# Kernel optimization log

Measured on AMD Instinct MI355X. Metric: run time of the kernel, lower is better.

Reference implementation:

```python
import jax, jax.numpy as jnp
import numpy as np

S = 14       # grid size
B = 2        # boxes per cell
C = 20       # classes
N_EL = B * 5 + C   # 30
L_COORD = 5.0
L_NOOBJ = 0.5
BATCH = 4096
NBOX = 16


def setup_inputs() -> dict:
    key = jax.random.key(0)
    k1, k2, k3, k4 = jax.random.split(key, 4)
    prediction = jax.random.uniform(k1, (BATCH, S * S * N_EL), dtype=jnp.float32)
    # well-formed ground-truth boxes: centers in (0.05,0.95), sizes in (0.02,0.3)
    cxcy = jax.random.uniform(k2, (BATCH, NBOX, 2), minval=0.05, maxval=0.95, dtype=jnp.float32)
    wh = jax.random.uniform(k3, (BATCH, NBOX, 2), minval=0.02, maxval=0.3, dtype=jnp.float32)
    boxes = jnp.concatenate([cxcy - wh / 2, cxcy + wh / 2], axis=-1)  # x1,y1,x2,y2
    classes = jax.random.randint(k4, (BATCH, NBOX), 0, C, dtype=jnp.int32)
    return {"prediction": prediction, "boxes": boxes, "classes": classes}


def _encode(boxes, classes):
    """Vectorized version of YoloLoss.encode: scatter boxes into SxS grid cells.
    Faithful detail: class one-hot goes to channel 9+class (the original's
    off-by-one: class 0 lands on the 2nd confidence channel)."""
    bsz, nbox = classes.shape
    cell = 1.0 / S
    xy1, xy2 = boxes[..., :2], boxes[..., 2:]
    wh = xy2 - xy1
    cxcy = (xy1 + xy2) / 2
    ij = jnp.clip(jnp.ceil(cxcy / cell) - 1, 0, S - 1)          # [b,nbox,2] (x,y)
    dxy = cxcy / cell - ij                                      # delta inside cell
    ij = ij.astype(jnp.int32)
    one = jnp.ones_like(wh[..., :1])
    zcls = jnp.zeros(classes.shape + (C,), dtype=boxes.dtype)
    # layout: [dxy, wh, conf, dxy, wh, conf, class one-hots]
    base = jnp.concatenate([dxy, wh, one, dxy, wh, one, zcls], axis=-1)  # [b,nbox,30]
    cls_oh = jax.nn.one_hot(classes + (B * 5 - 1), N_EL, dtype=boxes.dtype)  # index 9+class
    vec = jnp.maximum(base, cls_oh)
    flat_idx = (jnp.arange(bsz, dtype=jnp.int32)[:, None] * (S * S)
                + ij[..., 1] * S + ij[..., 0]).reshape(-1)      # row-major (y,x)
    target = jnp.zeros((bsz * S * S, N_EL), dtype=boxes.dtype)
    return target.at[flat_idx].set(vec.reshape(-1, N_EL))


def _pairwise_iou(a, b):
    """a,b: [N,B,4] -> iou [N,B(pred),B(target)] (corner-format jaccard, as in
    the original, applied to (dx,dy,w,h) rows verbatim)."""
    a4 = a[:, :, None, :]
    b4 = b[:, None, :, :]
    lt = jnp.maximum(a4[..., :2], b4[..., :2])
    rb = jnp.minimum(a4[..., 2:], b4[..., 2:])
    whi = jnp.clip(rb - lt, 0.0)
    inter = whi[..., 0] * whi[..., 1]
    area_a = (a4[..., 2] - a4[..., 0]) * (a4[..., 3] - a4[..., 1])
    area_b = (b4[..., 2] - b4[..., 0]) * (b4[..., 3] - b4[..., 1])
    union = area_a + area_b - inter
    return inter / jnp.where(union == 0, 1.0, union)


def reference(prediction, boxes, classes):
    target = _encode(boxes, classes)                       # [bsz*S*S, 30]
    pred = prediction.reshape(-1, N_EL)
    coord = target[:, 4] > 0                               # cells containing objects
    coordf = coord.astype(pred.dtype)
    noobjf = (target[:, 4] == 0).astype(pred.dtype)

    conf_idx = jnp.array([4, 9])
    noobj_loss = jnp.sum(noobjf[:, None] * (pred[:, conf_idx] - target[:, conf_idx]) ** 2)
    class_loss = jnp.sum(coordf[:, None] * (pred[:, B * 5:] - target[:, B * 5:]) ** 2)

    bp = pred[:, :B * 5].reshape(-1, B, 5)                 # [N,B,5]
    bt = target[:, :B * 5].reshape(-1, B, 5)

    iou = _pairwise_iou(bp[..., :4], bt[..., :4])          # [N,B,B]
    max_index = jnp.argmax(iou, axis=1)                    # best pred per target box
    response = (max_index[:, None, :] == jnp.arange(B)[None, :, None]).any(-1)  # [N,B]
    resp = response & coord[:, None]
    respf = resp.astype(pred.dtype)

    contain_loss = jnp.sum(respf * (bp[..., 4] - bt[..., 4]) ** 2)
    bt_wh = jnp.where(resp[..., None], bt[..., 2:4], 1.0)  # guard sqrt at masked cells
    loc_loss = jnp.sum(respf * (((bp[..., :2] - bt[..., :2]) ** 2).sum(-1)
                                + ((jnp.sqrt(bp[..., 2:4]) - jnp.sqrt(bt_wh)) ** 2).sum(-1)))

    return L_COORD * loc_loss + contain_loss + L_NOOBJ * noobj_loss + class_loss
```

## Files before the change

### kernel.cpp

```cpp
#include <hip/hip_runtime.h>


#define SGRID 14
#define CELLS 196
#define NEL 30
#define NBOX 16
#define PRED_PER_BATCH 5880
#define VEC_PER_ROW 1470
#define STREAM_ITERS 12
#define STREAM_TPB 256
#define STREAM_CHUNK (STREAM_ITERS * STREAM_TPB)
#define WIN_TILE (4 * CELLS + 4)

typedef float v4f __attribute__((ext_vector_type(4)));

__device__ __forceinline__ float channel_sq_terms(v4f v, int c0, int m0, int m1) {
    float loss = 0.0f;
    #pragma unroll
    for (int j = 0; j < 4; ++j) {
        int cj = c0 + j;
        bool str = cj >= 30;
        int cc = str ? cj - 30 : cj;
        int m  = str ? m1 : m0;
        unsigned amask = (m < 0) ? 0x210u : 0x3FFFFC00u;
        float scale    = (m < 0) ? 0.5f : 1.0f;
        float wgt = ((amask >> cc) & 1u) ? scale : 0.0f;
        loss = fmaf(wgt * v[j], v[j], loss);
    }
    return loss;
}

__global__ __launch_bounds__(256) void yolo_fused_kernel(
    const v4f*    __restrict__ pred4,
    const float4* __restrict__ boxes,
    const int*    __restrict__ classes,
    float* __restrict__ partials,
    int nvec, int nrows)
{
    __shared__ int   s_win[WIN_TILE];
    __shared__ float s_w4[4];

    const int tid = threadIdx.x;
    const int v0  = blockIdx.x * STREAM_CHUNK;
    const int r0  = v0 / VEC_PER_ROW;
    const float cellw = (float)(1.0 / 14.0);

    float4 bx; int cls = 0; bool has_box = false;
    int rr = tid >> 4, row = r0 + rr, k = tid & 15;
    if (tid < 4 * NBOX && row < nrows) {
        bx  = boxes[row * NBOX + k];
        cls = classes[row * NBOX + k];
        has_box = true;
    }
    #pragma unroll
    for (int i = 0; i < (WIN_TILE + STREAM_TPB - 1) / STREAM_TPB; ++i) {
        int idx = tid + i * STREAM_TPB;
        if (idx < WIN_TILE) s_win[idx] = -1;
    }
    __syncthreads();
    float dx, dy, bw, bh; int cell = 0;
    if (has_box) {
        bw = bx.z - bx.x;  bh = bx.w - bx.y;
        float cx = (bx.x + bx.z) * 0.5f, cy = (bx.y + bx.w) * 0.5f;
        float fx = cx / cellw, fy = cy / cellw;
        float fi = fminf(fmaxf(ceilf(fx) - 1.0f, 0.0f), 13.0f);
        float fj = fminf(fmaxf(ceilf(fy) - 1.0f, 0.0f), 13.0f);
        dx = fx - fi;  dy = fy - fj;
        cell = (int)fj * SGRID + (int)fi;
        atomicMax(&s_win[rr * CELLS + cell], (k << 8) | (9 + cls));
    }
    __syncthreads();

    const int cellbase = r0 * CELLS;
    float loss = 0.0f;
    if (v0 + STREAM_CHUNK <= nvec) {
        v4f vv[STREAM_ITERS];
        #pragma unroll
        for (int i = 0; i < STREAM_ITERS; ++i)
            vv[i] = pred4[v0 + tid + i * STREAM_TPB];
        int g0 = (v0 + tid) * 4;
        int c  = (int)((unsigned)g0 / 30u);
        int c0 = g0 - c * 30;
        int lc = c - cellbase;
        #pragma unroll
        for (int i = 0; i < STREAM_ITERS; ++i) {
            loss += channel_sq_terms(vv[i], c0, s_win[lc], s_win[lc + 1]);
            lc += 34;  c0 += 4;
            if (c0 >= 30) { c0 -= 30; lc += 1; }
        }
    } else {
        for (int i = 0; i < STREAM_ITERS; ++i) {
            int e = v0 + tid + i * STREAM_TPB;
            if (e < nvec) {
                v4f v = pred4[e];
                int g = e * 4;
                int c = (int)((unsigned)g / 30u);
                loss += channel_sq_terms(v, g - c * 30, s_win[c - cellbase],
                                         s_win[c - cellbase + 1]);
            }
        }
    }

    if (has_box) {
        int rstart = row * VEC_PER_ROW;
        if (rstart >= v0 && rstart < v0 + STREAM_CHUNK) {
            int wv = s_win[rr * CELLS + cell];
            if ((wv >> 8) == k) {
                const float* p = (const float*)pred4 + (size_t)(row * CELLS + cell) * NEL;
                int hot = wv & 0xFF;
                if (hot >= 10) loss += 1.0f - 2.0f * p[hot];
                float a[10];
                #pragma unroll
                for (int j = 0; j < 5; ++j) {
                    float2 v = *(const float2*)(p + 2 * j);
                    a[2 * j] = v.x;  a[2 * j + 1] = v.y;
                }
                float area_t = (bw - dx) * (bh - dy);
                float iou[2];
                #pragma unroll
                for (int i = 0; i < 2; ++i) {
                    const float* q = a + i * 5;
                    float ltx = fmaxf(q[0], dx), lty = fmaxf(q[1], dy);
                    float rbx = fminf(q[2], bw), rby = fminf(q[3], bh);
                    float wi = fmaxf(rbx - ltx, 0.0f);
                    float hi = fmaxf(rby - lty, 0.0f);
                    float inter  = wi * hi;
                    float area_a = (q[2] - q[0]) * (q[3] - q[1]);
                    float uni    = area_a + area_t - inter;
                    iou[i] = inter / ((uni == 0.0f) ? 1.0f : uni);
                }
                int r = (iou[1] > iou[0]) ? 1 : 0;
                const float* q = a + r * 5;
                float dc = q[4] - 1.0f;
                loss += dc * dc;
                float lx = q[0] - dx, ly = q[1] - dy;
                float lw = sqrtf(q[2]) - sqrtf(bw);
                float lh = sqrtf(q[3]) - sqrtf(bh);
                loss += 5.0f * (lx * lx + ly * ly + lw * lw + lh * lh);
            }
        }
    }

    #pragma unroll
    for (int off = 32; off > 0; off >>= 1)
        loss += __shfl_down(loss, off, 64);
    if ((tid & 63) == 0) s_w4[tid >> 6] = loss;
    __syncthreads();
    if (tid == 0)
        partials[blockIdx.x] = s_w4[0] + s_w4[1] + s_w4[2] + s_w4[3];
}

__global__ __launch_bounds__(1024) void final_reduce_kernel(
    const float* __restrict__ partials, float* __restrict__ out, int n)
{
    float s = 0.0f;
    #pragma unroll 2
    for (int i = threadIdx.x; i < n; i += 1024) s += partials[i];
    #pragma unroll
    for (int off = 32; off > 0; off >>= 1)
        s += __shfl_down(s, off, 64);
    __shared__ float w16[16];
    if ((threadIdx.x & 63) == 0) w16[threadIdx.x >> 6] = s;
    __syncthreads();
    if (threadIdx.x < 64) {
        float t = (threadIdx.x < 16) ? w16[threadIdx.x] : 0.0f;
        #pragma unroll
        for (int off = 8; off > 0; off >>= 1)
            t += __shfl_down(t, off, 64);
        if (threadIdx.x == 0) out[0] = t;
    }
}

extern "C" void kernel_launch(void* const* d_in, const int* in_sizes, int n_in,
                              void* d_out, int out_size, void* d_ws, size_t ws_size,
                              hipStream_t stream) {
    const float* pred    = (const float*)d_in[0];
    const float* boxes   = (const float*)d_in[1];
    const int*   classes = (const int*)d_in[2];
    float* out = (float*)d_out;

    const int nrows = in_sizes[0] / PRED_PER_BATCH;
    const int nvec  = nrows * PRED_PER_BATCH / 4;
    const int sblocks = (nvec + STREAM_CHUNK - 1) / STREAM_CHUNK;

    float* partials = (float*)d_ws;

    yolo_fused_kernel<<<dim3(sblocks), dim3(STREAM_TPB), 0, stream>>>(
        (const v4f*)pred, (const float4*)boxes, classes, partials, nvec, nrows);
    final_reduce_kernel<<<dim3(1), dim3(1024), 0, stream>>>(partials, out, sblocks);
}
```

Baseline: 144.5 us.

## Decouple object-cell work from streaming pass with uniform noobj weights and correction

Every element now gets a uniform 0.5 weight on channels 4 and 9 in the streaming pass, so the per-element shared-memory lookup of cell occupancy goes away. Object cells are handled separately by the first blocks, each covering 16 batch rows. These blocks add the class squared-error sum and subtract the noobj terms that were over-counted. The block-level shared reduction is replaced by per-wave partial writes, and the final reduction sums four times as many partials. The risk is load imbalance from the extra object work and its 16x196 shared tile on the first blocks.

```diff
diff --git a/kernel.cpp b/kernel.cpp
--- a/kernel.cpp
+++ b/kernel.cpp
@@ -10,111 +10,85 @@
 #define STREAM_ITERS 12
 #define STREAM_TPB 256
 #define STREAM_CHUNK (STREAM_ITERS * STREAM_TPB)
-#define WIN_TILE (4 * CELLS + 4)
+#define ROWS_PER_OBJ_BLOCK 16
+#define OBJ_TILE (ROWS_PER_OBJ_BLOCK * CELLS)
 
 typedef float v4f __attribute__((ext_vector_type(4)));
-
-__device__ __forceinline__ float channel_sq_terms(v4f v, int c0, int m0, int m1) {
-    float loss = 0.0f;
-    #pragma unroll
-    for (int j = 0; j < 4; ++j) {
-        int cj = c0 + j;
-        bool str = cj >= 30;
-        int cc = str ? cj - 30 : cj;
-        int m  = str ? m1 : m0;
-        unsigned amask = (m < 0) ? 0x210u : 0x3FFFFC00u;
-        float scale    = (m < 0) ? 0.5f : 1.0f;
-        float wgt = ((amask >> cc) & 1u) ? scale : 0.0f;
-        loss = fmaf(wgt * v[j], v[j], loss);
-    }
-    return loss;
-}
 
 __global__ __launch_bounds__(256) void yolo_fused_kernel(
     const v4f*    __restrict__ pred4,
     const float4* __restrict__ boxes,
     const int*    __restrict__ classes,
     float* __restrict__ partials,
-    int nvec, int nrows)
+    int nvec, int nrows, int objblocks)
 {
-    __shared__ int   s_win[WIN_TILE];
-    __shared__ float s_w4[4];
+    __shared__ int s_win[OBJ_TILE];
 
     const int tid = threadIdx.x;
-    const int v0  = blockIdx.x * STREAM_CHUNK;
-    const int r0  = v0 / VEC_PER_ROW;
+    const int bid = blockIdx.x;
+    const int v0  = bid * STREAM_CHUNK;
     const float cellw = (float)(1.0 / 14.0);
-
-    float4 bx; int cls = 0; bool has_box = false;
-    int rr = tid >> 4, row = r0 + rr, k = tid & 15;
-    if (tid < 4 * NBOX && row < nrows) {
+    const bool isobj = bid < objblocks;
+
+    float4 bx; int cls = 0;
+    const int row = bid * ROWS_PER_OBJ_BLOCK + (tid >> 4);
+    const int k   = tid & 15;
+    const bool has_box = isobj && row < nrows;
+    if (has_box) {
         bx  = boxes[row * NBOX + k];
         cls = classes[row * NBOX + k];
-        has_box = true;
-    }
-    #pragma unroll
-    for (int i = 0; i < (WIN_TILE + STREAM_TPB - 1) / STREAM_TPB; ++i) {
-        int idx = tid + i * STREAM_TPB;
-        if (idx < WIN_TILE) s_win[idx] = -1;
-    }
-    __syncthreads();
-    float dx, dy, bw, bh; int cell = 0;
-    if (has_box) {
-        bw = bx.z - bx.x;  bh = bx.w - bx.y;
-        float cx = (bx.x + bx.z) * 0.5f, cy = (bx.y + bx.w) * 0.5f;
-        float fx = cx / cellw, fy = cy / cellw;
-        float fi = fminf(fmaxf(ceilf(fx) - 1.0f, 0.0f), 13.0f);
-        float fj = fminf(fmaxf(ceilf(fy) - 1.0f, 0.0f), 13.0f);
-        dx = fx - fi;  dy = fy - fj;
-        cell = (int)fj * SGRID + (int)fi;
-        atomicMax(&s_win[rr * CELLS + cell], (k << 8) | (9 + cls));
-    }
-    __syncthreads();
-
-    const int cellbase = r0 * CELLS;
+    }
+
     float loss = 0.0f;
-    if (v0 + STREAM_CHUNK <= nvec) {
-        v4f vv[STREAM_ITERS];
+    const bool full = (v0 + STREAM_CHUNK) <= nvec;
+
+    v4f vv[STREAM_ITERS];
+    if (full) {
         #pragma unroll
         for (int i = 0; i < STREAM_ITERS; ++i)
             vv[i] = pred4[v0 + tid + i * STREAM_TPB];
-        int g0 = (v0 + tid) * 4;
-        int c  = (int)((unsigned)g0 / 30u);
-        int c0 = g0 - c * 30;
-        int lc = c - cellbase;
-        #pragma unroll
-        for (int i = 0; i < STREAM_ITERS; ++i) {
-            loss += channel_sq_terms(vv[i], c0, s_win[lc], s_win[lc + 1]);
-            lc += 34;  c0 += 4;
-            if (c0 >= 30) { c0 -= 30; lc += 1; }
-        }
-    } else {
-        for (int i = 0; i < STREAM_ITERS; ++i) {
-            int e = v0 + tid + i * STREAM_TPB;
-            if (e < nvec) {
-                v4f v = pred4[e];
-                int g = e * 4;
-                int c = (int)((unsigned)g / 30u);
-                loss += channel_sq_terms(v, g - c * 30, s_win[c - cellbase],
-                                         s_win[c - cellbase + 1]);
-            }
-        }
-    }
-
-    if (has_box) {
-        int rstart = row * VEC_PER_ROW;
-        if (rstart >= v0 && rstart < v0 + STREAM_CHUNK) {
-            int wv = s_win[rr * CELLS + cell];
+    }
+
+    if (isobj) {
+        #pragma unroll
+        for (int i = 0; i < (OBJ_TILE + STREAM_TPB - 1) / STREAM_TPB; ++i) {
+            int idx = tid + i * STREAM_TPB;
+            if (idx < OBJ_TILE) s_win[idx] = -1;
+        }
+        __syncthreads();
+        float dx, dy, bw, bh; int cell = 0;
+        if (has_box) {
+            bw = bx.z - bx.x;  bh = bx.w - bx.y;
+            float cx = (bx.x + bx.z) * 0.5f, cy = (bx.y + bx.w) * 0.5f;
+            float fx = cx / cellw, fy = cy / cellw;
+            float fi = fminf(fmaxf(ceilf(fx) - 1.0f, 0.0f), 13.0f);
+            float fj = fminf(fmaxf(ceilf(fy) - 1.0f, 0.0f), 13.0f);
+            dx = fx - fi;  dy = fy - fj;
+            cell = (int)fj * SGRID + (int)fi;
+            atomicMax(&s_win[(tid >> 4) * CELLS + cell], (k << 8) | (9 + cls));
+        }
+        __syncthreads();
+        if (has_box) {
+            int wv = s_win[(tid >> 4) * CELLS + cell];
             if ((wv >> 8) == k) {
                 const float* p = (const float*)pred4 + (size_t)(row * CELLS + cell) * NEL;
                 int hot = wv & 0xFF;
-                if (hot >= 10) loss += 1.0f - 2.0f * p[hot];
                 float a[10];
                 #pragma unroll
                 for (int j = 0; j < 5; ++j) {
-                    float2 v = *(const float2*)(p + 2 * j);
-                    a[2 * j] = v.x;  a[2 * j + 1] = v.y;
-                }
+                    float2 t = *(const float2*)(p + 2 * j);
+                    a[2 * j] = t.x;  a[2 * j + 1] = t.y;
+                }
+                float csum = 0.0f;
+                #pragma unroll
+                for (int j = 0; j < 10; ++j) {
+                    float2 t = *(const float2*)(p + 10 + 2 * j);
+                    float d0 = t.x - ((10 + 2 * j) == hot ? 1.0f : 0.0f);
+                    float d1 = t.y - ((11 + 2 * j) == hot ? 1.0f : 0.0f);
+                    csum += d0 * d0 + d1 * d1;
+                }
+                loss += csum;
+                loss -= 0.5f * (a[4] * a[4] + a[9] * a[9]);
                 float area_t = (bw - dx) * (bh - dy);
                 float iou[2];
                 #pragma unroll
@@ -141,20 +115,53 @@
         }
     }
 
+    if (full) {
+        int g0 = (v0 + tid) * 4;
+        int c  = (int)((unsigned)g0 / 30u);
+        int c0 = g0 - c * 30;
+        #pragma unroll
+        for (int i = 0; i < STREAM_ITERS; ++i) {
+            v4f v = vv[i];
+            #pragma unroll
+            for (int j = 0; j < 4; ++j) {
+                int cj = c0 + j;
+                int cc = (cj >= 30) ? cj - 30 : cj;
+                float wgt = ((cc == 4) | (cc == 9)) ? 0.5f : 0.0f;
+                loss = fmaf(wgt * v[j], v[j], loss);
+            }
+            c0 += 4;  if (c0 >= 30) c0 -= 30;
+        }
+    } else {
+        for (int i = 0; i < STREAM_ITERS; ++i) {
+            int e = v0 + tid + i * STREAM_TPB;
+            if (e < nvec) {
+                v4f v = pred4[e];
+                int g = e * 4;
+                int c = (int)((unsigned)g / 30u);
+                int c0 = g - c * 30;
+                #pragma unroll
+                for (int j = 0; j < 4; ++j) {
+                    int cj = c0 + j;
+                    int cc = (cj >= 30) ? cj - 30 : cj;
+                    float wgt = ((cc == 4) | (cc == 9)) ? 0.5f : 0.0f;
+                    loss = fmaf(wgt * v[j], v[j], loss);
+                }
+            }
+        }
+    }
+
     #pragma unroll
     for (int off = 32; off > 0; off >>= 1)
         loss += __shfl_down(loss, off, 64);
-    if ((tid & 63) == 0) s_w4[tid >> 6] = loss;
-    __syncthreads();
-    if (tid == 0)
-        partials[blockIdx.x] = s_w4[0] + s_w4[1] + s_w4[2] + s_w4[3];
+    if ((tid & 63) == 0)
+        partials[bid * 4 + (tid >> 6)] = loss;
 }
 
 __global__ __launch_bounds__(1024) void final_reduce_kernel(
     const float* __restrict__ partials, float* __restrict__ out, int n)
 {
     float s = 0.0f;
-    #pragma unroll 2
+    #pragma unroll 4
     for (int i = threadIdx.x; i < n; i += 1024) s += partials[i];
     #pragma unroll
     for (int off = 32; off > 0; off >>= 1)
@@ -181,11 +188,13 @@
 
     const int nrows = in_sizes[0] / PRED_PER_BATCH;
     const int nvec  = nrows * PRED_PER_BATCH / 4;
-    const int sblocks = (nvec + STREAM_CHUNK - 1) / STREAM_CHUNK;
+    const int sblocks   = (nvec + STREAM_CHUNK - 1) / STREAM_CHUNK;
+    const int objblocks = (nrows + ROWS_PER_OBJ_BLOCK - 1) / ROWS_PER_OBJ_BLOCK;
 
     float* partials = (float*)d_ws;
 
     yolo_fused_kernel<<<dim3(sblocks), dim3(STREAM_TPB), 0, stream>>>(
-        (const v4f*)pred, (const float4*)boxes, classes, partials, nvec, nrows);
-    final_reduce_kernel<<<dim3(1), dim3(1024), 0, stream>>>(partials, out, sblocks);
+        (const v4f*)pred, (const float4*)boxes, classes, partials,
+        nvec, nrows, objblocks);
+    final_reduce_kernel<<<dim3(1), dim3(1024), 0, stream>>>(partials, out, sblocks * 4);
 }
```

New measurement: 144.4 us. About the same (-0.0%).
